# Optimization experiments

Measured on AMD Instinct MI355X. Metric: run time of the kernel, lower is better.

Reference implementation:

```python
import jax, jax.numpy as jnp
import numpy as np

D_MODEL = 1
D_INNER = 2      # expand(2) * d_model
D_STATE = 16
D_CONV = 4
DT_RANK = 1      # ceil(d_model / 16)


def _mamba(u, in_proj_w, conv_w, conv_b, x_proj_w, dt_proj_w, dt_proj_b, A_log, Dp, out_proj_w):
    # u: [B, L, d_model]
    B, L, _ = u.shape
    d_inner, d_state = A_log.shape
    xz = u @ in_proj_w.T                          # [B, L, 2*d_inner]
    x, z = jnp.split(xz, 2, axis=-1)
    # causal depthwise conv over sequence
    xt = jnp.transpose(x, (0, 2, 1))              # [B, d_inner, L]
    xt = jax.lax.conv_general_dilated(
        xt, conv_w, window_strides=(1,), padding=[(D_CONV - 1, 0)],
        feature_group_count=d_inner, dimension_numbers=('NCH', 'OIH', 'NCH'))
    xt = xt + conv_b[None, :, None]
    x = jax.nn.silu(jnp.transpose(xt, (0, 2, 1)))  # [B, L, d_inner]
    x_dbl = x @ x_proj_w.T                        # [B, L, dt_rank + 2*d_state]
    dt, Bm, Cm = jnp.split(x_dbl, [DT_RANK, DT_RANK + d_state], axis=-1)
    dt = jax.nn.softplus(dt @ dt_proj_w.T + dt_proj_b)  # [B, L, d_inner]
    A = -jnp.exp(A_log)                           # [d_inner, d_state]
    dA = jnp.exp(dt[..., None] * A)               # [B, L, d_inner, d_state]
    dBu = dt[..., None] * Bm[:, :, None, :] * x[..., None]

    def step(h, inp):
        dA_t, dBu_t, C_t = inp                    # [B,d,s], [B,d,s], [B,s]
        h = dA_t * h + dBu_t
        y = jnp.einsum('bds,bs->bd', h, C_t)
        return h, y

    h0 = jnp.zeros((B, d_inner, d_state), dtype=u.dtype)
    xs = (jnp.moveaxis(dA, 1, 0), jnp.moveaxis(dBu, 1, 0), jnp.moveaxis(Cm, 1, 0))
    _, ys = jax.lax.scan(step, h0, xs)            # ys: [L, B, d_inner]
    y = jnp.moveaxis(ys, 0, 1) + x * Dp           # skip term D*x
    y = y * jax.nn.silu(z)                        # gated output
    return y @ out_proj_w.T                       # [B, L, d_model]


def setup_inputs() -> dict:
    key = jax.random.key(0)
    ks = jax.random.split(key, 12)
    B, H, W, C = 16, 64, 64, 512
    s = 0.1
    return {
        'x1': jax.random.normal(ks[0], (B, H, W, C), jnp.float32),
        'x2': jax.random.normal(ks[1], (B, H, W, C), jnp.float32),
        'in_proj_w': jax.random.normal(ks[2], (2 * D_INNER, D_MODEL), jnp.float32) * s,
        'conv_w': jax.random.normal(ks[3], (D_INNER, 1, D_CONV), jnp.float32) * s,
        'conv_b': jax.random.normal(ks[4], (D_INNER,), jnp.float32) * s,
        'x_proj_w': jax.random.normal(ks[5], (DT_RANK + 2 * D_STATE, D_INNER), jnp.float32) * s,
        'dt_proj_w': jax.random.normal(ks[6], (D_INNER, DT_RANK), jnp.float32) * s,
        'dt_proj_b': jax.random.normal(ks[7], (D_INNER,), jnp.float32) * s,
        'A_log': jnp.log(jnp.broadcast_to(jnp.arange(1, D_STATE + 1, dtype=jnp.float32), (D_INNER, D_STATE))),
        'Dp': jnp.ones((D_INNER,), jnp.float32),
        'out_proj_w': jax.random.normal(ks[8], (D_MODEL, D_INNER), jnp.float32) * s,
    }


def reference(x1, x2, in_proj_w, conv_w, conv_b, x_proj_w, dt_proj_w, dt_proj_b, A_log, Dp, out_proj_w):
    B, H, W, C = x1.shape
    pooled = jnp.mean(x1, axis=(1, 2))[..., None]   # GAP -> [B, C, 1]: seq len C, d_model 1
    att = _mamba(pooled, in_proj_w, conv_w, conv_b, x_proj_w,
                 dt_proj_w, dt_proj_b, A_log, Dp, out_proj_w)  # [B, C, 1]
    return x2 * att.reshape(B, 1, 1, C)
```

## Files before the change

### kernel.cpp

```cpp
#include <hip/hip_runtime.h>
#include <math.h>

#define BATCH   16
#define CH      512
#define HW      4096
#define NCHUNK  64
#define ROWS    (HW / NCHUNK)
#define DSTATE  16
#define SCHUNK  16
#define CLEN    (CH / SCHUNK)
#define APPU    8

typedef float f4 __attribute__((ext_vector_type(4)));

__device__ __forceinline__ float siluf(float x) {
    return x / (1.0f + expf(-x));
}
__device__ __forceinline__ float softplusf(float x) {
    return (x > 20.0f) ? x : log1pf(expf(x));
}

__global__ void __launch_bounds__(512) gap_partial(const f4* __restrict__ x1,
                                                   f4* __restrict__ partial) {
    int b     = blockIdx.x / NCHUNK;
    int chunk = blockIdx.x % NCHUNK;
    int t  = threadIdx.x;
    int c4 = t & 127;
    int rg = t >> 7;
    const f4* p = x1 + ((size_t)b * HW + (size_t)chunk * ROWS) * 128 + c4;
    f4 acc = (f4)(0.f);
    #pragma unroll
    for (int r = rg; r < ROWS; r += 4) {
        f4 v = __builtin_nontemporal_load(p + (size_t)r * 128);
        acc += v;
    }
    __shared__ f4 red[4][128];
    red[rg][c4] = acc;
    __syncthreads();
    if (rg == 0) {
        f4 s = red[0][c4] + red[1][c4] + red[2][c4] + red[3][c4];
        partial[(size_t)(chunk * BATCH + b) * 128 + c4] = s;
    }
}

__global__ void __launch_bounds__(512) mamba_fused(const float* __restrict__ partial,
                                                   const float* __restrict__ in_proj_w,
                                                   const float* __restrict__ conv_w,
                                                   const float* __restrict__ conv_b,
                                                   const float* __restrict__ x_proj_w,
                                                   const float* __restrict__ dt_proj_w,
                                                   const float* __restrict__ dt_proj_b,
                                                   const float* __restrict__ A_log,
                                                   const float* __restrict__ Dp,
                                                   const float* __restrict__ out_proj_w,
                                                   float* __restrict__ att)
{
    int b   = blockIdx.x;
    int tid = threadIdx.x;

    __shared__ float pool[CH];
    {
        float s = 0.f;
        #pragma unroll 8
        for (int k = 0; k < NCHUNK; ++k)
            s += partial[(size_t)k * (BATCH * CH) + b * CH + tid];
        pool[tid] = s * (1.0f / (float)HW);
    }
    __syncthreads();

    __shared__ float sx0[CH], sx1[CH], sdt0[CH], sdt1[CH], scf0[CH], scf1[CH], ssk[CH];
    {
        int l = tid;
        float u0  = pool[l];
        float um1 = (l >= 1) ? pool[l - 1] : 0.f;
        float um2 = (l >= 2) ? pool[l - 2] : 0.f;
        float um3 = (l >= 3) ? pool[l - 3] : 0.f;
        float xs[2], cf[2], dtv[2];
        #pragma unroll
        for (int d = 0; d < 2; ++d) {
            float conv = um3 * conv_w[d * 4 + 0] + um2 * conv_w[d * 4 + 1] +
                         um1 * conv_w[d * 4 + 2] + u0  * conv_w[d * 4 + 3];
            float xc = in_proj_w[d] * conv + conv_b[d];
            xs[d] = siluf(xc);
            float z = u0 * in_proj_w[2 + d];
            cf[d] = siluf(z) * out_proj_w[d];
        }
        float dt_raw = xs[0] * x_proj_w[0] + xs[1] * x_proj_w[1];
        #pragma unroll
        for (int d = 0; d < 2; ++d)
            dtv[d] = softplusf(dt_raw * dt_proj_w[d] + dt_proj_b[d]);
        sx0[l] = xs[0]; sx1[l] = xs[1];
        sdt0[l] = dtv[0]; sdt1[l] = dtv[1];
        scf0[l] = cf[0]; scf1[l] = cf[1];
        ssk[l] = xs[0] * Dp[0] * cf[0] + xs[1] * Dp[1] * cf[1];
    }
    __syncthreads();

    int ds    = tid & 31;
    int chunk = tid >> 5;
    int si    = ds & 15;
    int d     = ds >> 4;
    float Aval = -expf(A_log[d * DSTATE + si]);
    float wB0 = x_proj_w[(1 + si) * 2],  wB1 = x_proj_w[(1 + si) * 2 + 1];
    float wC0 = x_proj_w[(17 + si) * 2], wC1 = x_proj_w[(17 + si) * 2 + 1];
    const float* sdt = d ? sdt1 : sdt0;
    const float* scf = d ? scf1 : scf0;
    const float* sxd = d ? sx1  : sx0;

    float a_[CLEN], b_[CLEN], c_[CLEN];
    int l0 = chunk * CLEN;
    #pragma unroll
    for (int l = 0; l < CLEN; ++l) {
        int L = l0 + l;
        float x0 = sx0[L], x1v = sx1[L];
        float dt = sdt[L];
        float Bs = x0 * wB0 + x1v * wB1;
        float Cs = x0 * wC0 + x1v * wC1;
        a_[l] = expf(dt * Aval);
        b_[l] = dt * Bs * sxd[L];
        c_[l] = Cs * scf[L];
    }

    float P = 1.f, Q = 0.f;
    #pragma unroll
    for (int l = 0; l < CLEN; ++l) { P *= a_[l]; Q = fmaf(a_[l], Q, b_[l]); }

    __shared__ float sP[SCHUNK][32], sQ[SCHUNK][32];
    sP[chunk][ds] = P; sQ[chunk][ds] = Q;
    __syncthreads();
    float h = 0.f;
    for (int j = 0; j < chunk; ++j) h = fmaf(sP[j][ds], h, sQ[j][ds]);

    float* patt = att + (size_t)b * CH + l0;
    #pragma unroll
    for (int l = 0; l < CLEN; ++l) {
        h = fmaf(a_[l], h, b_[l]);
        float p = h * c_[l];
        p += __shfl_xor(p, 1, 32);
        p += __shfl_xor(p, 2, 32);
        p += __shfl_xor(p, 4, 32);
        p += __shfl_xor(p, 8, 32);
        p += __shfl_xor(p, 16, 32);
        if (ds == 0) patt[l] = ssk[l0 + l] + p;
    }
}

__global__ void __launch_bounds__(256) apply_att(const f4* __restrict__ x2,
                                                 const f4* __restrict__ att4,
                                                 f4* __restrict__ out)
{
    size_t base = (size_t)blockIdx.x * (256 * APPU) + threadIdx.x;
    f4 a = att4[((base >> 19) << 7) + (base & 127)];
    f4 v[APPU];
    #pragma unroll
    for (int k = 0; k < APPU; ++k)
        v[k] = __builtin_nontemporal_load(x2 + base + k * 256);
    #pragma unroll
    for (int k = 0; k < APPU; ++k)
        __builtin_nontemporal_store(v[k] * a, out + base + k * 256);
}

extern "C" void kernel_launch(void* const* d_in, const int* in_sizes, int n_in,
                              void* d_out, int out_size, void* d_ws, size_t ws_size,
                              hipStream_t stream) {
    const float* x1         = (const float*)d_in[0];
    const float* x2         = (const float*)d_in[1];
    const float* in_proj_w  = (const float*)d_in[2];
    const float* conv_w     = (const float*)d_in[3];
    const float* conv_b     = (const float*)d_in[4];
    const float* x_proj_w   = (const float*)d_in[5];
    const float* dt_proj_w  = (const float*)d_in[6];
    const float* dt_proj_b  = (const float*)d_in[7];
    const float* A_log      = (const float*)d_in[8];
    const float* Dp         = (const float*)d_in[9];
    const float* out_proj_w = (const float*)d_in[10];

    float* ws = (float*)d_ws;
    size_t o = 0;
    float* partial = ws + o; o += (size_t)NCHUNK * BATCH * CH;
    float* attv    = ws + o; o += BATCH * CH;
    (void)ws_size; (void)in_sizes; (void)n_in; (void)out_size;

    gap_partial<<<BATCH * NCHUNK, 512, 0, stream>>>((const f4*)x1, (f4*)partial);
    mamba_fused<<<BATCH, 512, 0, stream>>>(partial, in_proj_w, conv_w, conv_b,
                                           x_proj_w, dt_proj_w, dt_proj_b,
                                           A_log, Dp, out_proj_w, attv);
    int n4 = (BATCH * HW * CH) / 4;
    int nblk = n4 / (256 * APPU);
    apply_att<<<nblk, 256, 0, stream>>>((const f4*)x2, (const f4*)attv, (f4*)d_out);
}
```

Baseline: 84.96 us.

## Fuse GAP reduction and Mamba scan via last-block atomic counter

Merges the pooling partial-sum kernel and the Mamba scan kernel into one launch. The last block to finish for each batch, detected with an atomic counter and a threadfence, runs the scan. The scan also recomputes its per-step coefficients in both passes instead of holding them in register arrays, which lowers register pressure. This saves a kernel launch and lets scans for early-finishing batches overlap other blocks' reductions, at the cost of an extra memset and a 512-thread block carrying scan code paths.

```diff
diff --git a/kernel.cpp b/kernel.cpp
--- a/kernel.cpp
+++ b/kernel.cpp
@@ -20,44 +20,50 @@
     return (x > 20.0f) ? x : log1pf(expf(x));
 }
 
-__global__ void __launch_bounds__(512) gap_partial(const f4* __restrict__ x1,
-                                                   f4* __restrict__ partial) {
+__global__ void __launch_bounds__(512) gap_scan(const f4* __restrict__ x1,
+                                                f4* __restrict__ partial4,
+                                                int* __restrict__ cnt,
+                                                const float* __restrict__ in_proj_w,
+                                                const float* __restrict__ conv_w,
+                                                const float* __restrict__ conv_b,
+                                                const float* __restrict__ x_proj_w,
+                                                const float* __restrict__ dt_proj_w,
+                                                const float* __restrict__ dt_proj_b,
+                                                const float* __restrict__ A_log,
+                                                const float* __restrict__ Dp,
+                                                const float* __restrict__ out_proj_w,
+                                                float* __restrict__ att)
+{
     int b     = blockIdx.x / NCHUNK;
     int chunk = blockIdx.x % NCHUNK;
-    int t  = threadIdx.x;
-    int c4 = t & 127;
-    int rg = t >> 7;
+    int tid   = threadIdx.x;
+    int c4 = tid & 127;
+    int rg = tid >> 7;
+
     const f4* p = x1 + ((size_t)b * HW + (size_t)chunk * ROWS) * 128 + c4;
     f4 acc = (f4)(0.f);
     #pragma unroll
-    for (int r = rg; r < ROWS; r += 4) {
-        f4 v = __builtin_nontemporal_load(p + (size_t)r * 128);
-        acc += v;
-    }
+    for (int r = rg; r < ROWS; r += 4)
+        acc += __builtin_nontemporal_load(p + (size_t)r * 128);
     __shared__ f4 red[4][128];
     red[rg][c4] = acc;
     __syncthreads();
     if (rg == 0) {
         f4 s = red[0][c4] + red[1][c4] + red[2][c4] + red[3][c4];
-        partial[(size_t)(chunk * BATCH + b) * 128 + c4] = s;
-    }
-}
-
-__global__ void __launch_bounds__(512) mamba_fused(const float* __restrict__ partial,
-                                                   const float* __restrict__ in_proj_w,
-                                                   const float* __restrict__ conv_w,
-                                                   const float* __restrict__ conv_b,
-                                                   const float* __restrict__ x_proj_w,
-                                                   const float* __restrict__ dt_proj_w,
-                                                   const float* __restrict__ dt_proj_b,
-                                                   const float* __restrict__ A_log,
-                                                   const float* __restrict__ Dp,
-                                                   const float* __restrict__ out_proj_w,
-                                                   float* __restrict__ att)
-{
-    int b   = blockIdx.x;
-    int tid = threadIdx.x;
-
+        partial4[(size_t)(chunk * BATCH + b) * 128 + c4] = s;
+    }
+
+    __shared__ int last;
+    __syncthreads();
+    if (tid == 0) {
+        __threadfence();
+        last = (atomicAdd(cnt + b, 1) == NCHUNK - 1) ? 1 : 0;
+    }
+    __syncthreads();
+    if (!last) return;
+    __threadfence();
+
+    const float* partial = (const float*)partial4;
     __shared__ float pool[CH];
     {
         float s = 0.f;
@@ -97,7 +103,7 @@
     __syncthreads();
 
     int ds    = tid & 31;
-    int chunk = tid >> 5;
+    int schk  = tid >> 5;
     int si    = ds & 15;
     int d     = ds >> 4;
     float Aval = -expf(A_log[d * DSTATE + si]);
@@ -106,42 +112,44 @@
     const float* sdt = d ? sdt1 : sdt0;
     const float* scf = d ? scf1 : scf0;
     const float* sxd = d ? sx1  : sx0;
-
-    float a_[CLEN], b_[CLEN], c_[CLEN];
-    int l0 = chunk * CLEN;
-    #pragma unroll
+    int l0 = schk * CLEN;
+
+    float P = 1.f, Q = 0.f;
+    #pragma unroll 8
     for (int l = 0; l < CLEN; ++l) {
         int L = l0 + l;
-        float x0 = sx0[L], x1v = sx1[L];
         float dt = sdt[L];
-        float Bs = x0 * wB0 + x1v * wB1;
-        float Cs = x0 * wC0 + x1v * wC1;
-        a_[l] = expf(dt * Aval);
-        b_[l] = dt * Bs * sxd[L];
-        c_[l] = Cs * scf[L];
-    }
-
-    float P = 1.f, Q = 0.f;
-    #pragma unroll
-    for (int l = 0; l < CLEN; ++l) { P *= a_[l]; Q = fmaf(a_[l], Q, b_[l]); }
+        float Bs = sx0[L] * wB0 + sx1[L] * wB1;
+        float a  = expf(dt * Aval);
+        float bb = dt * Bs * sxd[L];
+        P *= a;
+        Q = fmaf(a, Q, bb);
+    }
 
     __shared__ float sP[SCHUNK][32], sQ[SCHUNK][32];
-    sP[chunk][ds] = P; sQ[chunk][ds] = Q;
+    sP[schk][ds] = P; sQ[schk][ds] = Q;
     __syncthreads();
     float h = 0.f;
-    for (int j = 0; j < chunk; ++j) h = fmaf(sP[j][ds], h, sQ[j][ds]);
+    for (int j = 0; j < schk; ++j) h = fmaf(sP[j][ds], h, sQ[j][ds]);
 
     float* patt = att + (size_t)b * CH + l0;
-    #pragma unroll
+    #pragma unroll 8
     for (int l = 0; l < CLEN; ++l) {
-        h = fmaf(a_[l], h, b_[l]);
-        float p = h * c_[l];
-        p += __shfl_xor(p, 1, 32);
-        p += __shfl_xor(p, 2, 32);
-        p += __shfl_xor(p, 4, 32);
-        p += __shfl_xor(p, 8, 32);
-        p += __shfl_xor(p, 16, 32);
-        if (ds == 0) patt[l] = ssk[l0 + l] + p;
+        int L = l0 + l;
+        float dt = sdt[L];
+        float Bs = sx0[L] * wB0 + sx1[L] * wB1;
+        float Cs = sx0[L] * wC0 + sx1[L] * wC1;
+        float a  = expf(dt * Aval);
+        float bb = dt * Bs * sxd[L];
+        float c  = Cs * scf[L];
+        h = fmaf(a, h, bb);
+        float pr = h * c;
+        pr += __shfl_xor(pr, 1, 32);
+        pr += __shfl_xor(pr, 2, 32);
+        pr += __shfl_xor(pr, 4, 32);
+        pr += __shfl_xor(pr, 8, 32);
+        pr += __shfl_xor(pr, 16, 32);
+        if (ds == 0) patt[l] = ssk[L] + pr;
     }
 }
 
@@ -179,12 +187,16 @@
     size_t o = 0;
     float* partial = ws + o; o += (size_t)NCHUNK * BATCH * CH;
     float* attv    = ws + o; o += BATCH * CH;
+    int*   cnt     = (int*)(ws + o); o += BATCH;
     (void)ws_size; (void)in_sizes; (void)n_in; (void)out_size;
 
-    gap_partial<<<BATCH * NCHUNK, 512, 0, stream>>>((const f4*)x1, (f4*)partial);
-    mamba_fused<<<BATCH, 512, 0, stream>>>(partial, in_proj_w, conv_w, conv_b,
-                                           x_proj_w, dt_proj_w, dt_proj_b,
-                                           A_log, Dp, out_proj_w, attv);
+    hipMemsetAsync(cnt, 0, BATCH * sizeof(int), stream);
+
+    gap_scan<<<BATCH * NCHUNK, 512, 0, stream>>>((const f4*)x1, (f4*)partial, cnt,
+                                                 in_proj_w, conv_w, conv_b,
+                                                 x_proj_w, dt_proj_w, dt_proj_b,
+                                                 A_log, Dp, out_proj_w, attv);
+
     int n4 = (BATCH * HW * CH) / 4;
     int nblk = n4 / (256 * APPU);
     apply_att<<<nblk, 256, 0, stream>>>((const f4*)x2, (const f4*)attv, (f4*)d_out);
```

Result: slower. 155.5 us (+83.0%).
